# Kernel optimization log

Hardware: AMD Instinct MI355X
Metric: run time of the kernel (lower is better)

Reference implementation:

```python
import jax, jax.numpy as jnp
import numpy as np

N = 50000   # nodes
E = 800000  # edges
D = 64      # dim_node
H = 64      # hidden_channels
G = 512     # graphs in batch


def setup_inputs() -> dict:
    key = jax.random.key(0)
    ks = jax.random.split(key, 13)
    s = 0.05
    return dict(
        x=jax.random.normal(ks[0], (N, D), jnp.float32),
        edge_index=jax.random.randint(ks[1], (2, E), 0, N, dtype=jnp.int32),
        batch_idx=jnp.sort(jax.random.randint(ks[2], (N,), 0, G, dtype=jnp.int32)),
        W0=jax.random.normal(ks[3], (D, H), jnp.float32) * s,
        b0=jnp.zeros((H,), jnp.float32),
        W1=jax.random.normal(ks[4], (H, H), jnp.float32) * s,
        b1=jnp.zeros((H,), jnp.float32),
        W2=jax.random.normal(ks[5], (H, H), jnp.float32) * s,
        b2=jnp.zeros((H,), jnp.float32),
        lin1_w=jax.random.normal(ks[6], (H, H), jnp.float32) * s,
        lin1_b=jnp.zeros((H,), jnp.float32),
        lin2_w=jax.random.normal(ks[7], (H, 1), jnp.float32) * s,
        lin2_b=jnp.zeros((1,), jnp.float32),
    )


def gcn_conv(x, W, b, src, dst, n):
    """PyG GCNConv: out = D^{-1/2} (A + I) D^{-1/2} X W + b (self-loops added)."""
    h = x @ W                                   # [n, H] transform first (cheaper)
    loop = jnp.arange(n, dtype=src.dtype)
    row = jnp.concatenate([src, loop])          # message sources (incl. self-loops)
    col = jnp.concatenate([dst, loop])          # aggregation targets
    deg = jax.ops.segment_sum(jnp.ones_like(col, jnp.float32), col, num_segments=n)
    dinv = jnp.where(deg > 0, jax.lax.rsqrt(deg), 0.0)
    norm = dinv[row] * dinv[col]                # [E+n]
    msg = h[row] * norm[:, None]                # gather + scale
    return jax.ops.segment_sum(msg, col, num_segments=n) + b


def reference(x, edge_index, batch_idx, W0, b0, W1, b1, W2, b2,
              lin1_w, lin1_b, lin2_w, lin2_b):
    src, dst = edge_index[0], edge_index[1]
    h = jax.nn.relu(gcn_conv(x, W0, b0, src, dst, N))   # dropout(p=0, eval) = identity
    h = jax.nn.relu(gcn_conv(h, W1, b1, src, dst, N))
    h = jax.nn.relu(gcn_conv(h, W2, b2, src, dst, N))
    # global_mean_pool over graph ids
    sums = jax.ops.segment_sum(h, batch_idx, num_segments=G)            # [G, H]
    cnt = jax.ops.segment_sum(jnp.ones((N,), jnp.float32), batch_idx, num_segments=G)
    pooled = sums / jnp.maximum(cnt, 1.0)[:, None]
    h = jax.nn.relu(pooled @ lin1_w + lin1_b)
    return h @ lin2_w + lin2_b                                          # [G, 1]
```

## Files before the change

### kernel.cpp

```cpp
#include <hip/hip_runtime.h>
#include <math.h>

#define NN 50000
#define EE 800000
#define HH 64
#define GG 512
#define SCAN_NB ((NN + 1023) / 1024)
#define NC 8

typedef unsigned short ushort_t;
typedef unsigned int uint_t;

__device__ __forceinline__ ushort_t f32_to_bf16(float f) {
    uint_t u = __float_as_uint(f);
    uint_t bias = 0x7FFFu + ((u >> 16) & 1u);
    return (ushort_t)((u + bias) >> 16);
}
__device__ __forceinline__ float bf16_to_f32(ushort_t h) {
    return __uint_as_float(((uint_t)h) << 16);
}


__global__ void k_deg(const int* __restrict__ dst, int* __restrict__ degc,
                      int* __restrict__ rank) {
    int e = blockIdx.x * blockDim.x + threadIdx.x;
    if (e < EE) {
        int c = (e >> 8) & (NC - 1);
        rank[e] = atomicAdd(&degc[c * NN + dst[e]], 1);
    }
}


__global__ void __launch_bounds__(1024) k_scan1(const int* __restrict__ degc,
                                                int* __restrict__ rowptr,
                                                int* __restrict__ bsum,
                                                uint4* __restrict__ off8,
                                                float* __restrict__ dinv) {
    int tid = threadIdx.x;
    int lane = tid & 63, w = tid >> 6;
    int i = blockIdx.x * 1024 + tid;
    int total = 0;
    int offv[NC];
#pragma unroll
    for (int c = 0; c < NC; ++c) {
        int dc = (i < NN) ? degc[c * NN + i] : 0;
        offv[c] = total;
        total += dc;
    }
    if (i < NN) {
        dinv[i] = 1.0f / sqrtf((float)(total + 1));
        off8[i] = make_uint4((uint_t)offv[0] | ((uint_t)offv[1] << 16),
                             (uint_t)offv[2] | ((uint_t)offv[3] << 16),
                             (uint_t)offv[4] | ((uint_t)offv[5] << 16),
                             (uint_t)offv[6] | ((uint_t)offv[7] << 16));
    } else if (i == NN) {
        dinv[i] = 0.0f;
    }
    int v = (i < NN) ? total : 0;
    int x = v;
#pragma unroll
    for (int off = 1; off < 64; off <<= 1) {
        int y = __shfl_up(x, off);
        if (lane >= off) x += y;
    }
    __shared__ int ws[16];
    if (lane == 63) ws[w] = x;
    __syncthreads();
    if (tid < 16) {
        int y = ws[tid];
        int z = y;
#pragma unroll
        for (int off = 1; off < 16; off <<= 1) {
            int t2 = __shfl_up(z, off);
            if (tid >= off) z += t2;
        }
        ws[tid] = z - y;
    }
    __syncthreads();
    int excl = x - v + ws[w];
    if (i <= NN) rowptr[i] = excl;
    if (tid == 1023) bsum[blockIdx.x] = excl + v;
}

__global__ void __launch_bounds__(64) k_scan2(int* __restrict__ bsum) {
    int lane = threadIdx.x;
    int v = (lane < SCAN_NB) ? bsum[lane] : 0;
    int x = v;
#pragma unroll
    for (int off = 1; off < 64; off <<= 1) {
        int y = __shfl_up(x, off);
        if (lane >= off) x += y;
    }
    if (lane < SCAN_NB) bsum[lane] = x - v;
}


__global__ void k_base(const int* __restrict__ rowptr, const int* __restrict__ bsum,
                       const uint4* __restrict__ off8,
                       int* __restrict__ rowptr_abs, int* __restrict__ base8) {
    int i = blockIdx.x * blockDim.x + threadIdx.x;
    if (i > NN) return;
    int base = rowptr[i] + bsum[i >> 10];
    rowptr_abs[i] = base;
    if (i < NN) {
        uint4 pk = off8[i];
        base8[0 * NN + i] = base + (int)(pk.x & 0xFFFFu);
        base8[1 * NN + i] = base + (int)(pk.x >> 16);
        base8[2 * NN + i] = base + (int)(pk.y & 0xFFFFu);
        base8[3 * NN + i] = base + (int)(pk.y >> 16);
        base8[4 * NN + i] = base + (int)(pk.z & 0xFFFFu);
        base8[5 * NN + i] = base + (int)(pk.z >> 16);
        base8[6 * NN + i] = base + (int)(pk.w & 0xFFFFu);
        base8[7 * NN + i] = base + (int)(pk.w >> 16);
    }
}


__global__ void k_fill(const int* __restrict__ src, const int* __restrict__ dst,
                       const int* __restrict__ rank, const int* __restrict__ base8,
                       const int* __restrict__ batch,
                       ushort_t* __restrict__ csr_src, int* __restrict__ cnt) {
    int tid = blockIdx.x * blockDim.x + threadIdx.x;
    if (tid < EE) {
        int d = dst[tid];
        int c = (tid >> 8) & (NC - 1);
        csr_src[base8[c * NN + d] + rank[tid]] = (ushort_t)src[tid];
    } else if (tid < EE + NN) {
        atomicAdd(&cnt[batch[tid - EE]], 1);
    }
}


template<bool RELU>
__global__ void __launch_bounds__(256) k_xform(const float* __restrict__ x,
                                               const float* __restrict__ W,
                                               const float* __restrict__ dinv,
                                               ushort_t* __restrict__ t) {
    __shared__ float sW[64 * 64];
    __shared__ float sX[32 * 65];
    int tid = threadIdx.x;
    for (int k = tid; k < 64 * 64; k += 256) sW[k] = W[k];
    int row0 = blockIdx.x * 32;
    for (int v = tid; v < 32 * 16; v += 256) {
        int r  = v >> 4;
        int k4 = (v & 15) * 4;
        int row = row0 + r;
        float4 val = make_float4(0.f, 0.f, 0.f, 0.f);
        if (row < NN) val = *(const float4*)(x + (size_t)row * 64 + k4);
        if (RELU) {
            val.x = fmaxf(val.x, 0.f); val.y = fmaxf(val.y, 0.f);
            val.z = fmaxf(val.z, 0.f); val.w = fmaxf(val.w, 0.f);
        }
        sX[r * 65 + k4 + 0] = val.x;
        sX[r * 65 + k4 + 1] = val.y;
        sX[r * 65 + k4 + 2] = val.z;
        sX[r * 65 + k4 + 3] = val.w;
    }
    __syncthreads();
    int r  = tid >> 3;
    int c0 = (tid & 7) * 8;
    float acc[8] = {0.f, 0.f, 0.f, 0.f, 0.f, 0.f, 0.f, 0.f};
    for (int k = 0; k < 64; ++k) {
        float xv = sX[r * 65 + k];
#pragma unroll
        for (int j = 0; j < 8; ++j) acc[j] = fmaf(xv, sW[k * 64 + c0 + j], acc[j]);
    }
    int row = row0 + r;
    if (row <= NN) {
        float dv = dinv[row];
        uint_t pk[4];
#pragma unroll
        for (int j = 0; j < 4; ++j) {
            ushort_t lo = f32_to_bf16(acc[2 * j] * dv);
            ushort_t hi = f32_to_bf16(acc[2 * j + 1] * dv);
            pk[j] = (uint_t)lo | ((uint_t)hi << 16);
        }
        uint4* o = (uint4*)(t + (size_t)row * 64 + c0);
        *o = make_uint4(pk[0], pk[1], pk[2], pk[3]);
    }
}


template<bool POOL>
__global__ void __launch_bounds__(256) k_gather(const ushort_t* __restrict__ t,
                                                const float* __restrict__ dinv,
                                                const int* __restrict__ rowptr_abs,
                                                const ushort_t* __restrict__ csr_src,
                                                const float* __restrict__ b,
                                                const int* __restrict__ batch,
                                                float* __restrict__ out) {
    int i = __builtin_amdgcn_readfirstlane((blockIdx.x * blockDim.x + threadIdx.x) >> 6);
    int c = threadIdx.x & 63;
    if (i >= NN) return;
    int e   = __builtin_amdgcn_readfirstlane(rowptr_abs[i]);
    int end = __builtin_amdgcn_readfirstlane(rowptr_abs[i + 1]);
    float acc = bf16_to_f32(t[(size_t)i * 64 + c]);
    float a0 = 0.f, a1 = 0.f, a2 = 0.f, a3 = 0.f;
    for (; e < end; e += 16) {
        int s[16];
#pragma unroll
        for (int j = 0; j < 16; ++j) {
            int sj = (int)csr_src[e + j];
            s[j] = (e + j < end) ? sj : NN;
        }
        ushort_t v[16];
#pragma unroll
        for (int j = 0; j < 16; ++j) v[j] = t[(size_t)s[j] * 64 + c];
#pragma unroll
        for (int j = 0; j < 16; ++j) {
            float f = bf16_to_f32(v[j]);
            if ((j & 3) == 0)      a0 += f;
            else if ((j & 3) == 1) a1 += f;
            else if ((j & 3) == 2) a2 += f;
            else                   a3 += f;
        }
    }
    acc += (a0 + a1) + (a2 + a3);
    float r = fmaf(acc, dinv[i], b[c]);
    if (POOL) {
        atomicAdd(&out[(size_t)batch[i] * 64 + c], fmaxf(r, 0.0f));
    } else {
        out[(size_t)i * 64 + c] = r;
    }
}


__global__ void __launch_bounds__(64) k_head(const float* __restrict__ pooled,
                                             const int* __restrict__ cnt,
                                             const float* __restrict__ w1,
                                             const float* __restrict__ b1,
                                             const float* __restrict__ w2,
                                             const float* __restrict__ b2,
                                             float* __restrict__ out) {
    int g = blockIdx.x;
    int c = threadIdx.x;
    __shared__ float sp[64];
    float cf = fmaxf((float)cnt[g], 1.0f);
    sp[c] = pooled[(size_t)g * 64 + c] / cf;
    __syncthreads();
    float acc = b1[c];
    for (int k = 0; k < 64; ++k) acc = fmaf(sp[k], w1[k * 64 + c], acc);
    float h1 = fmaxf(acc, 0.0f);
    float p = h1 * w2[c];
#pragma unroll
    for (int off = 32; off > 0; off >>= 1) p += __shfl_down(p, off);
    if (c == 0) out[g] = p + b2[0];
}


extern "C" void kernel_launch(void* const* d_in, const int* in_sizes, int n_in,
                              void* d_out, int out_size, void* d_ws, size_t ws_size,
                              hipStream_t stream) {
    const float* x      = (const float*)d_in[0];
    const int*   ei     = (const int*)d_in[1];
    const int*   batch  = (const int*)d_in[2];
    const float* W0     = (const float*)d_in[3];
    const float* b0     = (const float*)d_in[4];
    const float* W1     = (const float*)d_in[5];
    const float* b1     = (const float*)d_in[6];
    const float* W2     = (const float*)d_in[7];
    const float* b2     = (const float*)d_in[8];
    const float* lin1w  = (const float*)d_in[9];
    const float* lin1b  = (const float*)d_in[10];
    const float* lin2w  = (const float*)d_in[11];
    const float* lin2b  = (const float*)d_in[12];
    float* out = (float*)d_out;

    const int* src = ei;
    const int* dst = ei + EE;

    char* ws = (char*)d_ws;
    size_t off = 0;
    auto carve = [&](size_t bytes) {
        void* p = ws + off;
        off = (off + bytes + 255) & ~(size_t)255;
        return p;
    };
    int*      degc     = (int*)carve((size_t)NC * NN * 4);
    float*    pooled   = (float*)carve((size_t)GG * 64 * 4);
    int*      cnt      = (int*)carve((size_t)GG * 4);
    size_t zero_span = off;
    float*    dinv     = (float*)carve((size_t)(NN + 1) * 4);
    int*      rowptr   = (int*)carve((size_t)(NN + 1) * 4);
    int*      bsum     = (int*)carve((size_t)SCAN_NB * 4);
    uint4*    off8     = (uint4*)carve((size_t)NN * 16);
    int*      rowptr_abs = (int*)carve((size_t)(NN + 1) * 4);
    int*      base8    = (int*)carve((size_t)NC * NN * 4);
    int*      rank     = (int*)carve((size_t)EE * 4);
    ushort_t* csr_src  = (ushort_t*)carve((size_t)(EE + 16) * 2);
    ushort_t* bufT     = (ushort_t*)carve((size_t)(NN + 1) * 64 * 2);
    float*    bufA     = (float*)carve((size_t)NN * 64 * 4);

    hipMemsetAsync(degc, 0, zero_span, stream);

    k_deg  <<<EE / 256, 256, 0, stream>>>(dst, degc, rank);
    k_scan1<<<SCAN_NB, 1024, 0, stream>>>(degc, rowptr, bsum, off8, dinv);
    k_scan2<<<1, 64, 0, stream>>>(bsum);
    k_base <<<(NN + 256) / 256, 256, 0, stream>>>(rowptr, bsum, off8, rowptr_abs, base8);
    k_fill <<<(EE + NN + 255) / 256, 256, 0, stream>>>(src, dst, rank, base8,
                                                       batch, csr_src, cnt);

    const int xgrid = (NN + 1 + 31) / 32;
    const int ggrid = (NN * 64) / 256;

    k_xform<false><<<xgrid, 256, 0, stream>>>(x, W0, dinv, bufT);
    k_gather<false><<<ggrid, 256, 0, stream>>>(bufT, dinv, rowptr_abs, csr_src,
                                               b0, batch, bufA);
    k_xform<true><<<xgrid, 256, 0, stream>>>(bufA, W1, dinv, bufT);
    k_gather<false><<<ggrid, 256, 0, stream>>>(bufT, dinv, rowptr_abs, csr_src,
                                               b1, batch, bufA);
    k_xform<true><<<xgrid, 256, 0, stream>>>(bufA, W2, dinv, bufT);
    k_gather<true><<<ggrid, 256, 0, stream>>>(bufT, dinv, rowptr_abs, csr_src,
                                              b2, batch, pooled);

    k_head<<<GG, 64, 0, stream>>>(pooled, cnt, lin1w, lin1b, lin2w, lin2b, out);
}
```

Baseline: 320.5 us.

## Gather two bf16 channels per lane across split-wave edges; fold scan2 into k_base

The gather kernel now splits each 64-lane wave into two halves. Each lane loads a 32-bit word holding two bf16 channels, and the two halves take alternating edges, so a wave processes 32 edges per iteration and the halves are combined with a cross-half shuffle. The intent is to use wider loads and fewer load instructions per edge in the memory-bound neighbour gather, at the cost of a shuffle reduction and only half the lanes writing output. Separately, the single-wave block-sum scan kernel is merged into k_base, with each block redoing the small scan in shared memory to save one launch. The padding of the CSR source array grows to cover the 32-wide edge reads.

Measured after the change: 512.7 us. 1.6x slower.

```diff
diff --git a/kernel.cpp b/kernel.cpp
--- a/kernel.cpp
+++ b/kernel.cpp
@@ -82,25 +82,28 @@
     if (tid == 1023) bsum[blockIdx.x] = excl + v;
 }
 
-__global__ void __launch_bounds__(64) k_scan2(int* __restrict__ bsum) {
-    int lane = threadIdx.x;
-    int v = (lane < SCAN_NB) ? bsum[lane] : 0;
-    int x = v;
-#pragma unroll
-    for (int off = 1; off < 64; off <<= 1) {
-        int y = __shfl_up(x, off);
-        if (lane >= off) x += y;
-    }
-    if (lane < SCAN_NB) bsum[lane] = x - v;
-}
-
-
-__global__ void k_base(const int* __restrict__ rowptr, const int* __restrict__ bsum,
-                       const uint4* __restrict__ off8,
-                       int* __restrict__ rowptr_abs, int* __restrict__ base8) {
-    int i = blockIdx.x * blockDim.x + threadIdx.x;
+
+__global__ void __launch_bounds__(256) k_base(const int* __restrict__ rowptr,
+                                              const int* __restrict__ bsum,
+                                              const uint4* __restrict__ off8,
+                                              int* __restrict__ rowptr_abs,
+                                              int* __restrict__ base8) {
+    __shared__ int sb[SCAN_NB];
+    int tid = threadIdx.x;
+    if (tid < 64) {
+        int v = (tid < SCAN_NB) ? bsum[tid] : 0;
+        int x = v;
+#pragma unroll
+        for (int off = 1; off < 64; off <<= 1) {
+            int y = __shfl_up(x, off);
+            if (tid >= off) x += y;
+        }
+        if (tid < SCAN_NB) sb[tid] = x - v;
+    }
+    __syncthreads();
+    int i = blockIdx.x * blockDim.x + tid;
     if (i > NN) return;
-    int base = rowptr[i] + bsum[i >> 10];
+    int base = rowptr[i] + sb[i >> 10];
     rowptr_abs[i] = base;
     if (i < NN) {
         uint4 pk = off8[i];
@@ -190,37 +193,49 @@
                                                 const int* __restrict__ batch,
                                                 float* __restrict__ out) {
     int i = __builtin_amdgcn_readfirstlane((blockIdx.x * blockDim.x + threadIdx.x) >> 6);
-    int c = threadIdx.x & 63;
+    int lane = threadIdx.x & 63;
+    int li   = lane & 31;
+    int half = lane >> 5;
     if (i >= NN) return;
     int e   = __builtin_amdgcn_readfirstlane(rowptr_abs[i]);
     int end = __builtin_amdgcn_readfirstlane(rowptr_abs[i + 1]);
-    float acc = bf16_to_f32(t[(size_t)i * 64 + c]);
-    float a0 = 0.f, a1 = 0.f, a2 = 0.f, a3 = 0.f;
-    for (; e < end; e += 16) {
-        int s[16];
-#pragma unroll
-        for (int j = 0; j < 16; ++j) {
+    float ax0 = 0.f, ay0 = 0.f, ax1 = 0.f, ay1 = 0.f;
+    for (; e < end; e += 32) {
+        int s[32];
+#pragma unroll
+        for (int j = 0; j < 32; ++j) {
             int sj = (int)csr_src[e + j];
             s[j] = (e + j < end) ? sj : NN;
         }
-        ushort_t v[16];
-#pragma unroll
-        for (int j = 0; j < 16; ++j) v[j] = t[(size_t)s[j] * 64 + c];
+        uint_t v[16];
+#pragma unroll
+        for (int j = 0; j < 16; ++j)
+            v[j] = *(const uint_t*)(t + (size_t)s[2 * j + half] * 64 + li * 2);
 #pragma unroll
         for (int j = 0; j < 16; ++j) {
-            float f = bf16_to_f32(v[j]);
-            if ((j & 3) == 0)      a0 += f;
-            else if ((j & 3) == 1) a1 += f;
-            else if ((j & 3) == 2) a2 += f;
-            else                   a3 += f;
-        }
-    }
-    acc += (a0 + a1) + (a2 + a3);
-    float r = fmaf(acc, dinv[i], b[c]);
-    if (POOL) {
-        atomicAdd(&out[(size_t)batch[i] * 64 + c], fmaxf(r, 0.0f));
-    } else {
-        out[(size_t)i * 64 + c] = r;
+            float fx = bf16_to_f32((ushort_t)(v[j] & 0xFFFFu));
+            float fy = bf16_to_f32((ushort_t)(v[j] >> 16));
+            if (j & 1) { ax1 += fx; ay1 += fy; }
+            else       { ax0 += fx; ay0 += fy; }
+        }
+    }
+    float ax = ax0 + ax1, ay = ay0 + ay1;
+    ax += __shfl_xor(ax, 32);
+    ay += __shfl_xor(ay, 32);
+    uint_t sp = *(const uint_t*)(t + (size_t)i * 64 + li * 2);
+    ax += bf16_to_f32((ushort_t)(sp & 0xFFFFu));
+    ay += bf16_to_f32((ushort_t)(sp >> 16));
+    float dv = dinv[i];
+    float rx = fmaf(ax, dv, b[li * 2 + 0]);
+    float ry = fmaf(ay, dv, b[li * 2 + 1]);
+    if (half == 0) {
+        if (POOL) {
+            float* p = &out[(size_t)batch[i] * 64 + li * 2];
+            atomicAdd(p + 0, fmaxf(rx, 0.f));
+            atomicAdd(p + 1, fmaxf(ry, 0.f));
+        } else {
+            *(float2*)(out + (size_t)i * 64 + li * 2) = make_float2(rx, ry);
+        }
     }
 }
 
@@ -287,7 +302,7 @@
     int*      rowptr_abs = (int*)carve((size_t)(NN + 1) * 4);
     int*      base8    = (int*)carve((size_t)NC * NN * 4);
     int*      rank     = (int*)carve((size_t)EE * 4);
-    ushort_t* csr_src  = (ushort_t*)carve((size_t)(EE + 16) * 2);
+    ushort_t* csr_src  = (ushort_t*)carve((size_t)(EE + 32) * 2);
     ushort_t* bufT     = (ushort_t*)carve((size_t)(NN + 1) * 64 * 2);
     float*    bufA     = (float*)carve((size_t)NN * 64 * 4);
 
@@ -295,8 +310,8 @@
 
     k_deg  <<<EE / 256, 256, 0, stream>>>(dst, degc, rank);
     k_scan1<<<SCAN_NB, 1024, 0, stream>>>(degc, rowptr, bsum, off8, dinv);
-    k_scan2<<<1, 64, 0, stream>>>(bsum);
-    k_base <<<(NN + 256) / 256, 256, 0, stream>>>(rowptr, bsum, off8, rowptr_abs, base8);
+    k_base <<<(NN + 1 + 255) / 256, 256, 0, stream>>>(rowptr, bsum, off8,
+                                                      rowptr_abs, base8);
     k_fill <<<(EE + NN + 255) / 256, 256, 0, stream>>>(src, dst, rank, base8,
                                                        batch, csr_src, cnt);
 
```
